# Kernel tuning notes

Measured on AMD Instinct MI355X. Metric: run time of the kernel, lower is better.

Reference implementation:

```python
import jax, jax.numpy as jnp
import numpy as np

NUM_NODES = 2048   # N (spatial)
SEQ_LEN = 512      # T (temporal)
LATENT = 32
LAYERS = 2
SELF_LOOP_EPS = 0.5
B = 4


def setup_inputs() -> dict:
    key = jax.random.key(0)
    k1, k2, k3 = jax.random.split(key, 3)
    NT = NUM_NODES + SEQ_LEN
    X = jax.random.normal(k1, (B, NT, LATENT), dtype=jnp.float32)
    # GraphSAGE-style per-layer weights: self and neighbor transforms + bias
    Ws = jax.random.normal(k2, (LAYERS, LATENT, LATENT), dtype=jnp.float32) * 0.05
    Wn = jax.random.normal(k3, (LAYERS, LATENT, LATENT), dtype=jnp.float32) * 0.05
    b = jnp.zeros((LAYERS, LATENT), dtype=jnp.float32)
    return {"X": X, "Ws": Ws, "Wn": Wn, "b": b}


def build_adj(X):
    # node_embs = concat(spatial, temporal) == X itself
    adj = jnp.einsum('bnf,bmf->bnm', X, X)          # [B, N+T, N+T]
    adj = jnp.tanh(jax.nn.relu(adj))
    NT = X.shape[1]
    adj = adj + SELF_LOOP_EPS * jnp.eye(NT, dtype=adj.dtype)
    return adj


def reference(X, Ws, Wn, b):
    adj = build_adj(X)
    h = X
    # dense weighted aggregation == sparse message passing over nonzero edges,
    # since edge weights are exactly the adjacency values
    for l in range(LAYERS):
        agg = jnp.einsum('bnm,bmd->bnd', adj, h)    # neighbor aggregation
        h = jax.nn.elu(jnp.einsum('bnd,de->bne', h, Ws[l])
                       + jnp.einsum('bnd,de->bne', agg, Wn[l])
                       + b[l])
    return h
```

## Files before the change

kernel.cpp:

```cpp
#include <hip/hip_runtime.h>
#include <math.h>

#define NT 2560
#define DF 32
#define NB 4
#define SELF_EPS 0.5f
#define MS 8
#define MROWS (NT / MS)
#define MT 64
#define MITERS (MROWS / MT)
#define TN 64
#define NBK (NT / TN)

typedef __attribute__((ext_vector_type(8))) short bf16x8;
typedef __attribute__((ext_vector_type(4))) float f32x4;

__device__ __forceinline__ unsigned pk2(float a, float b) {
    unsigned r;
    asm("v_cvt_pk_bf16_f32 %0, %1, %2" : "=v"(r) : "v"(a), "v"(b));
    return r;
}

__device__ __forceinline__ float fast_rcp(float x) {
#if __has_builtin(__builtin_amdgcn_rcpf)
    return __builtin_amdgcn_rcpf(x);
#else
    return 1.0f / x;
#endif
}

__device__ __forceinline__ float tanh_relu(float x) {
    x = fmaxf(x, 0.0f);
    float e = __expf(x + x);
    return 1.0f - 2.0f * fast_rcp(e + 1.0f);
}

__global__ __launch_bounds__(256, 4)
void prep(const float* __restrict__ X,
          unsigned short* __restrict__ Xb, unsigned short* __restrict__ XT)
{
    const int t = threadIdx.x;
    __shared__ float sT[32][33];
    const int tile = blockIdx.x;
    const int b = tile / 80, n0 = (tile % 80) * 32;
    const int row = t >> 3, c4 = (t & 7) * 4;
    const size_t rbase = ((size_t)(b * NT + n0 + row)) * DF + c4;
    const float4 v = *(const float4*)(X + rbase);
    unsigned p0 = pk2(v.x, v.y);
    unsigned p1 = pk2(v.z, v.w);
    *(uint2*)(Xb + rbase) = make_uint2(p0, p1);
    sT[row][c4 + 0] = v.x; sT[row][c4 + 1] = v.y;
    sT[row][c4 + 2] = v.z; sT[row][c4 + 3] = v.w;
    __syncthreads();
    const int d = t >> 3, nq = (t & 7) * 4;
    unsigned q0 = pk2(sT[nq + 0][d], sT[nq + 1][d]);
    unsigned q1 = pk2(sT[nq + 2][d], sT[nq + 3][d]);
    *(uint2*)(XT + ((size_t)(b * DF + d)) * NT + n0 + nq) = make_uint2(q0, q1);
}

__global__ __launch_bounds__(256, 4)
void gsage_main(const unsigned short* __restrict__ Xb,
                const unsigned short* __restrict__ HT,
                float* __restrict__ P,
                unsigned short* __restrict__ Sg)
{
    __shared__ unsigned short XmL[64 * 40];
    __shared__ unsigned short HtL[32 * 72];
    __shared__ unsigned short Ss[4 * 16 * 72];

    const int t = threadIdx.x;
    const int w = t >> 6, lane = t & 63;
    const int q = lane >> 4, c = lane & 15;
    const int n0 = blockIdx.x * TN;
    const int mbase = blockIdx.y * MROWS;
    const int b = blockIdx.z;

    const size_t xbase = (size_t)b * NT * DF;
    const size_t tbase = (size_t)b * DF * NT;

    const bf16x8 bfn = *(const bf16x8*)(Xb + xbase + (size_t)(n0 + w * 16 + c) * DF + q * 8);

    f32x4 acc0 = {0.f, 0.f, 0.f, 0.f};
    f32x4 acc1 = {0.f, 0.f, 0.f, 0.f};

    const int xrow = t >> 2, xseg = t & 3;
    const int hrow = t >> 3, hseg = t & 7;

    uint4 xv = *(const uint4*)(Xb + xbase + (size_t)(mbase + xrow) * DF + xseg * 8);
    uint4 hv = *(const uint4*)(HT + tbase + (size_t)hrow * NT + mbase + hseg * 8);

    const int n_g = n0 + w * 16 + c;
    unsigned short* SsW = Ss + w * (16 * 72);

    unsigned short* Sgw = Sg
        + ((((size_t)b * MS + blockIdx.y) * NBK + blockIdx.x) * 4 + w)
          * ((size_t)MITERS * 2 * 64 * 8)
        + (size_t)lane * 8;

    for (int it = 0; it < MITERS; ++it) {
        const int m0 = mbase + it * MT;
        __syncthreads();
        *(uint4*)(XmL + xrow * 40 + xseg * 8) = xv;
        *(uint4*)(HtL + hrow * 72 + hseg * 8) = hv;
        if (it + 1 < MITERS) {
            const int m1 = m0 + MT;
            xv = *(const uint4*)(Xb + xbase + (size_t)(m1 + xrow) * DF + xseg * 8);
            hv = *(const uint4*)(HT + tbase + (size_t)hrow * NT + m1 + hseg * 8);
        }
        __syncthreads();

        if (m0 == n0) {
            #pragma unroll
            for (int t4 = 0; t4 < 4; ++t4) {
                const bf16x8 af = *(const bf16x8*)(XmL + (t4 * 16 + c) * 40 + q * 8);
                const f32x4 zero = {0.f, 0.f, 0.f, 0.f};
                f32x4 st = __builtin_amdgcn_mfma_f32_16x16x32_bf16(af, bfn, zero, 0, 0, 0);
                const int m2 = m0 + t4 * 16 + q * 4;
                float v0 = tanh_relu(st[0]); if (n_g == m2 + 0) v0 += SELF_EPS;
                float v1 = tanh_relu(st[1]); if (n_g == m2 + 1) v1 += SELF_EPS;
                float v2 = tanh_relu(st[2]); if (n_g == m2 + 2) v2 += SELF_EPS;
                float v3 = tanh_relu(st[3]); if (n_g == m2 + 3) v3 += SELF_EPS;
                unsigned p0 = pk2(v0, v1);
                unsigned p1 = pk2(v2, v3);
                *(uint2*)(SsW + c * 72 + t4 * 16 + q * 4) = make_uint2(p0, p1);
            }
        } else {
            #pragma unroll
            for (int t4 = 0; t4 < 4; ++t4) {
                const bf16x8 af = *(const bf16x8*)(XmL + (t4 * 16 + c) * 40 + q * 8);
                const f32x4 zero = {0.f, 0.f, 0.f, 0.f};
                f32x4 st = __builtin_amdgcn_mfma_f32_16x16x32_bf16(af, bfn, zero, 0, 0, 0);
                unsigned p0 = pk2(tanh_relu(st[0]), tanh_relu(st[1]));
                unsigned p1 = pk2(tanh_relu(st[2]), tanh_relu(st[3]));
                *(uint2*)(SsW + c * 72 + t4 * 16 + q * 4) = make_uint2(p0, p1);
            }
        }
        asm volatile("s_waitcnt lgkmcnt(0)" ::: "memory");

        #pragma unroll
        for (int kc = 0; kc < 2; ++kc) {
            const bf16x8 sf = *(const bf16x8*)(SsW + c * 72 + kc * 32 + q * 8);
            *(uint4*)(Sgw + (size_t)(it * 2 + kc) * (64 * 8)) = __builtin_bit_cast(uint4, sf);
            const bf16x8 h0 = *(const bf16x8*)(HtL + c * 72 + kc * 32 + q * 8);
            const bf16x8 h1 = *(const bf16x8*)(HtL + (16 + c) * 72 + kc * 32 + q * 8);
            acc0 = __builtin_amdgcn_mfma_f32_16x16x32_bf16(sf, h0, acc0, 0, 0, 0);
            acc1 = __builtin_amdgcn_mfma_f32_16x16x32_bf16(sf, h1, acc1, 0, 0, 0);
        }
    }

    float* ap = P + ((size_t)blockIdx.y * NB + b) * NT * DF
                  + (size_t)(n0 + w * 16 + q * 4) * DF + c;
    #pragma unroll
    for (int r = 0; r < 4; ++r) {
        ap[(size_t)r * DF] = acc0[r];
        ap[(size_t)r * DF + 16] = acc1[r];
    }
}

__global__ __launch_bounds__(256, 6)
void gsage_agg(const unsigned short* __restrict__ Sg,
               const unsigned short* __restrict__ HT,
               float* __restrict__ P)
{
    __shared__ unsigned short HtL[32 * 72];

    const int t = threadIdx.x;
    const int w = t >> 6, lane = t & 63;
    const int q = lane >> 4, c = lane & 15;
    const int n0 = blockIdx.x * TN;
    const int mbase = blockIdx.y * MROWS;
    const int b = blockIdx.z;
    const size_t tbase = (size_t)b * DF * NT;

    const int hrow = t >> 3, hseg = t & 7;
    uint4 hv = *(const uint4*)(HT + tbase + (size_t)hrow * NT + mbase + hseg * 8);

    const unsigned short* Sp = Sg
        + ((((size_t)b * MS + blockIdx.y) * NBK + blockIdx.x) * 4 + w)
          * ((size_t)MITERS * 2 * 64 * 8)
        + (size_t)lane * 8;

    bf16x8 sf0 = *(const bf16x8*)(Sp);
    bf16x8 sf1 = *(const bf16x8*)(Sp + 64 * 8);

    f32x4 acc0 = {0.f, 0.f, 0.f, 0.f};
    f32x4 acc1 = {0.f, 0.f, 0.f, 0.f};

    for (int it = 0; it < MITERS; ++it) {
        __syncthreads();
        *(uint4*)(HtL + hrow * 72 + hseg * 8) = hv;
        bf16x8 nsf0, nsf1;
        if (it + 1 < MITERS) {
            hv = *(const uint4*)(HT + tbase + (size_t)hrow * NT
                                 + (mbase + (it + 1) * MT) + hseg * 8);
            nsf0 = *(const bf16x8*)(Sp + (size_t)((it + 1) * 2 + 0) * (64 * 8));
            nsf1 = *(const bf16x8*)(Sp + (size_t)((it + 1) * 2 + 1) * (64 * 8));
        }
        __syncthreads();

        const bf16x8 h00 = *(const bf16x8*)(HtL + c * 72 + 0 * 32 + q * 8);
        const bf16x8 h01 = *(const bf16x8*)(HtL + (16 + c) * 72 + 0 * 32 + q * 8);
        acc0 = __builtin_amdgcn_mfma_f32_16x16x32_bf16(sf0, h00, acc0, 0, 0, 0);
        acc1 = __builtin_amdgcn_mfma_f32_16x16x32_bf16(sf0, h01, acc1, 0, 0, 0);
        const bf16x8 h10 = *(const bf16x8*)(HtL + c * 72 + 1 * 32 + q * 8);
        const bf16x8 h11 = *(const bf16x8*)(HtL + (16 + c) * 72 + 1 * 32 + q * 8);
        acc0 = __builtin_amdgcn_mfma_f32_16x16x32_bf16(sf1, h10, acc0, 0, 0, 0);
        acc1 = __builtin_amdgcn_mfma_f32_16x16x32_bf16(sf1, h11, acc1, 0, 0, 0);

        if (it + 1 < MITERS) { sf0 = nsf0; sf1 = nsf1; }
    }

    float* ap = P + ((size_t)blockIdx.y * NB + b) * NT * DF
                  + (size_t)(n0 + w * 16 + q * 4) * DF + c;
    #pragma unroll
    for (int r = 0; r < 4; ++r) {
        ap[(size_t)r * DF] = acc0[r];
        ap[(size_t)r * DF + 16] = acc1[r];
    }
}

__global__ __launch_bounds__(256, 4)
void gsage_epi(const float* __restrict__ Hin, const float* __restrict__ P,
               const float* __restrict__ Wsl, const float* __restrict__ Wnl,
               const float* __restrict__ bl,
               float* __restrict__ Hout, unsigned short* __restrict__ HTout)
{
    __shared__ float sW[32][33], sN[32][33], sH[32][36], sA[32][36], sT[32][33];
    const int t = threadIdx.x;
    const int n0 = blockIdx.x * 32;
    const int b = blockIdx.y;
    const int row = t >> 3, c4 = (t & 7) * 4;
    const size_t rb = ((size_t)(b * NT + n0 + row)) * DF + c4;
    const float4 hv = *(const float4*)(Hin + rb);
    const size_t pstride = (size_t)NB * NT * DF;
    float4 av = *(const float4*)(P + rb);
    #pragma unroll
    for (int s = 1; s < MS; ++s) {
        const float4 pv = *(const float4*)(P + (size_t)s * pstride + rb);
        av.x += pv.x; av.y += pv.y; av.z += pv.z; av.w += pv.w;
    }
    const float4 w0 = *(const float4*)(Wsl + row * DF + c4);
    const float4 w1 = *(const float4*)(Wnl + row * DF + c4);
    sH[row][c4+0]=hv.x; sH[row][c4+1]=hv.y; sH[row][c4+2]=hv.z; sH[row][c4+3]=hv.w;
    sA[row][c4+0]=av.x; sA[row][c4+1]=av.y; sA[row][c4+2]=av.z; sA[row][c4+3]=av.w;
    sW[row][c4+0]=w0.x; sW[row][c4+1]=w0.y; sW[row][c4+2]=w0.z; sW[row][c4+3]=w0.w;
    sN[row][c4+0]=w1.x; sN[row][c4+1]=w1.y; sN[row][c4+2]=w1.z; sN[row][c4+3]=w1.w;
    __syncthreads();

    float4 z = make_float4(bl[c4+0], bl[c4+1], bl[c4+2], bl[c4+3]);
    #pragma unroll
    for (int k = 0; k < DF; ++k) {
        const float hk = sH[row][k], ak = sA[row][k];
        z.x += hk * sW[k][c4+0] + ak * sN[k][c4+0];
        z.y += hk * sW[k][c4+1] + ak * sN[k][c4+1];
        z.z += hk * sW[k][c4+2] + ak * sN[k][c4+2];
        z.w += hk * sW[k][c4+3] + ak * sN[k][c4+3];
    }
    z.x = z.x > 0.f ? z.x : __expf(z.x) - 1.f;
    z.y = z.y > 0.f ? z.y : __expf(z.y) - 1.f;
    z.z = z.z > 0.f ? z.z : __expf(z.z) - 1.f;
    z.w = z.w > 0.f ? z.w : __expf(z.w) - 1.f;
    *(float4*)(Hout + rb) = z;

    if (HTout != nullptr) {
        sT[row][c4+0]=z.x; sT[row][c4+1]=z.y; sT[row][c4+2]=z.z; sT[row][c4+3]=z.w;
        __syncthreads();
        const int d = t >> 3, nq = (t & 7) * 4;
        unsigned q0 = pk2(sT[nq+0][d], sT[nq+1][d]);
        unsigned q1 = pk2(sT[nq+2][d], sT[nq+3][d]);
        *(uint2*)(HTout + ((size_t)(b * DF + d)) * NT + n0 + nq) = make_uint2(q0, q1);
    }
}

extern "C" void kernel_launch(void* const* d_in, const int* in_sizes, int n_in,
                              void* d_out, int out_size, void* d_ws, size_t ws_size,
                              hipStream_t stream) {
    const float* X  = (const float*)d_in[0];
    const float* Ws = (const float*)d_in[1];
    const float* Wn = (const float*)d_in[2];
    const float* bv = (const float*)d_in[3];
    float* out = (float*)d_out;

    char* ws = (char*)d_ws;
    float* P  = (float*)ws;
    float* h1 = P + (size_t)MS * NB * NT * DF;
    unsigned short* Xb  = (unsigned short*)(ws + 11796480);
    unsigned short* XT  = Xb + (size_t)NB * NT * DF;
    unsigned short* H1T = XT + (size_t)NB * NT * DF;
    unsigned short* Sg  = H1T + (size_t)NB * NT * DF;

    prep<<<320, 256, 0, stream>>>(X, Xb, XT);

    dim3 g(NBK, MS, NB);
    gsage_main<<<g, 256, 0, stream>>>(Xb, XT, P, Sg);
    gsage_epi<<<dim3(NT / 32, NB), 256, 0, stream>>>(X, P, Ws, Wn, bv, h1, H1T);
    gsage_agg<<<g, 256, 0, stream>>>(Sg, H1T, P);
    gsage_epi<<<dim3(NT / 32, NB), 256, 0, stream>>>(h1, P, Ws + DF * DF, Wn + DF * DF,
                                                     bv + DF, out, nullptr);
}
```

Baseline: 99.70 us.

## Load MFMA operands directly from global memory instead of LDS staging

Removes the shared-memory staging of X and H tiles, and the two block barriers per iteration, in both the main and aggregation kernels. Each wave now reads its MFMA operand fragments straight from global memory, relying on L1/L2 caching. The aggregation loop is fully unrolled so loads can be issued early, and the launch-bounds occupancy targets are raised. The risk is redundant global/L2 traffic, since each wave re-reads the same fragments, and the loss of the explicit register prefetch.

```diff
diff --git a/kernel.cpp b/kernel.cpp
--- a/kernel.cpp
+++ b/kernel.cpp
@@ -58,14 +58,12 @@
     *(uint2*)(XT + ((size_t)(b * DF + d)) * NT + n0 + nq) = make_uint2(q0, q1);
 }
 
-__global__ __launch_bounds__(256, 4)
+__global__ __launch_bounds__(256, 6)
 void gsage_main(const unsigned short* __restrict__ Xb,
                 const unsigned short* __restrict__ HT,
                 float* __restrict__ P,
                 unsigned short* __restrict__ Sg)
 {
-    __shared__ unsigned short XmL[64 * 40];
-    __shared__ unsigned short HtL[32 * 72];
     __shared__ unsigned short Ss[4 * 16 * 72];
 
     const int t = threadIdx.x;
@@ -83,12 +81,6 @@
     f32x4 acc0 = {0.f, 0.f, 0.f, 0.f};
     f32x4 acc1 = {0.f, 0.f, 0.f, 0.f};
 
-    const int xrow = t >> 2, xseg = t & 3;
-    const int hrow = t >> 3, hseg = t & 7;
-
-    uint4 xv = *(const uint4*)(Xb + xbase + (size_t)(mbase + xrow) * DF + xseg * 8);
-    uint4 hv = *(const uint4*)(HT + tbase + (size_t)hrow * NT + mbase + hseg * 8);
-
     const int n_g = n0 + w * 16 + c;
     unsigned short* SsW = Ss + w * (16 * 72);
 
@@ -99,20 +91,13 @@
 
     for (int it = 0; it < MITERS; ++it) {
         const int m0 = mbase + it * MT;
-        __syncthreads();
-        *(uint4*)(XmL + xrow * 40 + xseg * 8) = xv;
-        *(uint4*)(HtL + hrow * 72 + hseg * 8) = hv;
-        if (it + 1 < MITERS) {
-            const int m1 = m0 + MT;
-            xv = *(const uint4*)(Xb + xbase + (size_t)(m1 + xrow) * DF + xseg * 8);
-            hv = *(const uint4*)(HT + tbase + (size_t)hrow * NT + m1 + hseg * 8);
-        }
-        __syncthreads();
+        asm volatile("s_waitcnt lgkmcnt(0)" ::: "memory");
 
         if (m0 == n0) {
             #pragma unroll
             for (int t4 = 0; t4 < 4; ++t4) {
-                const bf16x8 af = *(const bf16x8*)(XmL + (t4 * 16 + c) * 40 + q * 8);
+                const bf16x8 af = *(const bf16x8*)(Xb + xbase
+                    + (size_t)(m0 + t4 * 16 + c) * DF + q * 8);
                 const f32x4 zero = {0.f, 0.f, 0.f, 0.f};
                 f32x4 st = __builtin_amdgcn_mfma_f32_16x16x32_bf16(af, bfn, zero, 0, 0, 0);
                 const int m2 = m0 + t4 * 16 + q * 4;
@@ -127,7 +112,8 @@
         } else {
             #pragma unroll
             for (int t4 = 0; t4 < 4; ++t4) {
-                const bf16x8 af = *(const bf16x8*)(XmL + (t4 * 16 + c) * 40 + q * 8);
+                const bf16x8 af = *(const bf16x8*)(Xb + xbase
+                    + (size_t)(m0 + t4 * 16 + c) * DF + q * 8);
                 const f32x4 zero = {0.f, 0.f, 0.f, 0.f};
                 f32x4 st = __builtin_amdgcn_mfma_f32_16x16x32_bf16(af, bfn, zero, 0, 0, 0);
                 unsigned p0 = pk2(tanh_relu(st[0]), tanh_relu(st[1]));
@@ -141,8 +127,10 @@
         for (int kc = 0; kc < 2; ++kc) {
             const bf16x8 sf = *(const bf16x8*)(SsW + c * 72 + kc * 32 + q * 8);
             *(uint4*)(Sgw + (size_t)(it * 2 + kc) * (64 * 8)) = __builtin_bit_cast(uint4, sf);
-            const bf16x8 h0 = *(const bf16x8*)(HtL + c * 72 + kc * 32 + q * 8);
-            const bf16x8 h1 = *(const bf16x8*)(HtL + (16 + c) * 72 + kc * 32 + q * 8);
+            const bf16x8 h0 = *(const bf16x8*)(HT + tbase
+                + (size_t)c * NT + m0 + kc * 32 + q * 8);
+            const bf16x8 h1 = *(const bf16x8*)(HT + tbase
+                + (size_t)(16 + c) * NT + m0 + kc * 32 + q * 8);
             acc0 = __builtin_amdgcn_mfma_f32_16x16x32_bf16(sf, h0, acc0, 0, 0, 0);
             acc1 = __builtin_amdgcn_mfma_f32_16x16x32_bf16(sf, h1, acc1, 0, 0, 0);
         }
@@ -157,13 +145,11 @@
     }
 }
 
-__global__ __launch_bounds__(256, 6)
+__global__ __launch_bounds__(256, 8)
 void gsage_agg(const unsigned short* __restrict__ Sg,
                const unsigned short* __restrict__ HT,
                float* __restrict__ P)
 {
-    __shared__ unsigned short HtL[32 * 72];
-
     const int t = threadIdx.x;
     const int w = t >> 6, lane = t & 63;
     const int q = lane >> 4, c = lane & 15;
@@ -172,42 +158,27 @@
     const int b = blockIdx.z;
     const size_t tbase = (size_t)b * DF * NT;
 
-    const int hrow = t >> 3, hseg = t & 7;
-    uint4 hv = *(const uint4*)(HT + tbase + (size_t)hrow * NT + mbase + hseg * 8);
-
     const unsigned short* Sp = Sg
         + ((((size_t)b * MS + blockIdx.y) * NBK + blockIdx.x) * 4 + w)
           * ((size_t)MITERS * 2 * 64 * 8)
         + (size_t)lane * 8;
 
-    bf16x8 sf0 = *(const bf16x8*)(Sp);
-    bf16x8 sf1 = *(const bf16x8*)(Sp + 64 * 8);
-
     f32x4 acc0 = {0.f, 0.f, 0.f, 0.f};
     f32x4 acc1 = {0.f, 0.f, 0.f, 0.f};
 
+    #pragma unroll
     for (int it = 0; it < MITERS; ++it) {
-        __syncthreads();
-        *(uint4*)(HtL + hrow * 72 + hseg * 8) = hv;
-        bf16x8 nsf0, nsf1;
-        if (it + 1 < MITERS) {
-            hv = *(const uint4*)(HT + tbase + (size_t)hrow * NT
-                                 + (mbase + (it + 1) * MT) + hseg * 8);
-            nsf0 = *(const bf16x8*)(Sp + (size_t)((it + 1) * 2 + 0) * (64 * 8));
-            nsf1 = *(const bf16x8*)(Sp + (size_t)((it + 1) * 2 + 1) * (64 * 8));
+        const int m0 = mbase + it * MT;
+        #pragma unroll
+        for (int kc = 0; kc < 2; ++kc) {
+            const bf16x8 sf = *(const bf16x8*)(Sp + (size_t)(it * 2 + kc) * (64 * 8));
+            const bf16x8 h0 = *(const bf16x8*)(HT + tbase
+                + (size_t)c * NT + m0 + kc * 32 + q * 8);
+            const bf16x8 h1 = *(const bf16x8*)(HT + tbase
+                + (size_t)(16 + c) * NT + m0 + kc * 32 + q * 8);
+            acc0 = __builtin_amdgcn_mfma_f32_16x16x32_bf16(sf, h0, acc0, 0, 0, 0);
+            acc1 = __builtin_amdgcn_mfma_f32_16x16x32_bf16(sf, h1, acc1, 0, 0, 0);
         }
-        __syncthreads();
-
-        const bf16x8 h00 = *(const bf16x8*)(HtL + c * 72 + 0 * 32 + q * 8);
-        const bf16x8 h01 = *(const bf16x8*)(HtL + (16 + c) * 72 + 0 * 32 + q * 8);
-        acc0 = __builtin_amdgcn_mfma_f32_16x16x32_bf16(sf0, h00, acc0, 0, 0, 0);
-        acc1 = __builtin_amdgcn_mfma_f32_16x16x32_bf16(sf0, h01, acc1, 0, 0, 0);
-        const bf16x8 h10 = *(const bf16x8*)(HtL + c * 72 + 1 * 32 + q * 8);
-        const bf16x8 h11 = *(const bf16x8*)(HtL + (16 + c) * 72 + 1 * 32 + q * 8);
-        acc0 = __builtin_amdgcn_mfma_f32_16x16x32_bf16(sf1, h10, acc0, 0, 0, 0);
-        acc1 = __builtin_amdgcn_mfma_f32_16x16x32_bf16(sf1, h11, acc1, 0, 0, 0);
-
-        if (it + 1 < MITERS) { sf0 = nsf0; sf1 = nsf1; }
     }
 
     float* ap = P + ((size_t)blockIdx.y * NB + b) * NT * DF
```

Result: slower. 112.9 us (+13.2%).
